# Kernel optimization log

Measured on AMD Instinct MI355X. Metric: run time of the kernel, lower is better.

The kernel has to match this reference:

```python
import jax, jax.numpy as jnp
import numpy as np

N, E, H, R, C = 20000, 640000, 256, 10, 7
B, MAXLEN = 64, 110


def setup_inputs() -> dict:
    key = jax.random.key(0)
    ks = jax.random.split(key, 12)
    return {
        "speaker": jax.random.randint(ks[0], (N,), 0, 2),
        "x": jax.random.normal(ks[1], (N, H), dtype=jnp.float32),
        "edge_index": jax.random.randint(ks[2], (2, E), 0, N),
        "edge_norm": jax.random.uniform(ks[3], (E,), dtype=jnp.float32),
        "edge_type": jax.random.randint(ks[4], (E,), 0, R),
        "seq_lengths": jax.random.randint(ks[5], (B,), 1, MAXLEN),
        "umask": jnp.ones((B, MAXLEN), dtype=jnp.float32),
        "w1": jax.random.normal(ks[6], (R, H, H), dtype=jnp.float32) * 0.02,
        "w2": jax.random.normal(ks[7], (R, H, H), dtype=jnp.float32) * 0.02,
        "lin_W": jax.random.normal(ks[8], (2 * H, H), dtype=jnp.float32) * 0.02,
        "lin_b": jnp.zeros((H,), dtype=jnp.float32),
        "fc_W": jax.random.normal(ks[9], (H, C), dtype=jnp.float32) * 0.02,
        "fc_b": jnp.zeros((C,), dtype=jnp.float32),
    }


def gnn_layer(x, w, edge_index, edge_type, edge_norm):
    # PyG MessagePassing with flow='target_to_source', aggr='mean':
    #   x_j = x[edge_index[1]], aggregate at i = edge_index[0]
    i, j = edge_index[0], edge_index[1]
    # per-edge msg = x_j @ w[edge_type]; compute as relation-batched GEMM
    xw = jnp.einsum('nd,rdo->rno', x, w)          # [R, N, H]
    msgs = xw[edge_type, j] * edge_norm[:, None]   # [E, H]
    sums = jax.ops.segment_sum(msgs, i, num_segments=x.shape[0])
    cnt = jax.ops.segment_sum(jnp.ones_like(edge_norm), i, num_segments=x.shape[0])
    return sums / jnp.maximum(cnt, 1.0)[:, None]   # scatter-mean (0 for isolated nodes)


def reference(speaker, x, edge_index, edge_norm, edge_type, seq_lengths, umask,
              w1, w2, lin_W, lin_b, fc_W, fc_b):
    en = edge_norm * 2.0  # forward passes edge_norm * 2
    # both GNN layers are type 'GGCN' -> update() returns aggr_out (GRU path is dead)
    out1 = jax.nn.sigmoid(gnn_layer(x, w1, edge_index, edge_type, en))  # dropout = eval identity
    out2 = gnn_layer(out1, w2, edge_index, edge_type, en)
    emotions = jnp.concatenate([x, out2], axis=1)            # [N, 2H]
    hidden = jax.nn.relu(emotions @ lin_W + lin_b)           # [N, H]
    logits = hidden @ fc_W + fc_b                            # [N, C]
    log_prob = jax.nn.log_softmax(logits, axis=1)
    return (log_prob, x, emotions)
```

## Files before the change

kernel.cpp:

```cpp
#include <hip/hip_runtime.h>

typedef short bf16x8 __attribute__((ext_vector_type(8)));
typedef float f32x4 __attribute__((ext_vector_type(4)));

#define RH 2560

__device__ __forceinline__ unsigned short f2bf(float f) {
  unsigned u = __float_as_uint(f);
  u += 0x7fffu + ((u >> 16) & 1u);
  return (unsigned short)(u >> 16);
}
__device__ __forceinline__ float bf2f(unsigned short s) {
  return __uint_as_float(((unsigned)s) << 16);
}

__global__ void zero_int(int* __restrict__ p, int n) {
  int i = blockIdx.x * 256 + threadIdx.x;
  if (i < n) p[i] = 0;
}
__global__ void hist_kernel(const int* __restrict__ ei, int E, int* __restrict__ cnt) {
  int e = blockIdx.x * 256 + threadIdx.x;
  if (e < E) atomicAdd(&cnt[ei[e]], 1);
}
__global__ __launch_bounds__(1024) void scan_excl(const int* __restrict__ cnt,
                                                  int* __restrict__ offs, int n) {
  __shared__ int ps[1024];
  const int t = threadIdx.x;
  const int PER = (n + 1023) >> 10;
  const int base = t * PER;
  int s = 0;
  for (int k = 0; k < PER; ++k) {
    int idx = base + k;
    if (idx < n) s += cnt[idx];
  }
  ps[t] = s;
  __syncthreads();
  for (int off = 1; off < 1024; off <<= 1) {
    int add = (t >= off) ? ps[t - off] : 0;
    __syncthreads();
    ps[t] += add;
    __syncthreads();
  }
  int run = t ? ps[t - 1] : 0;
  for (int k = 0; k < PER; ++k) {
    int idx = base + k;
    if (idx < n) { offs[idx] = run; run += cnt[idx]; }
  }
  if (t == 1023) offs[n] = run;
}
__global__ void copy_int(const int* __restrict__ a, int* __restrict__ b, int n) {
  int i = blockIdx.x * 256 + threadIdx.x;
  if (i < n) b[i] = a[i];
}
__global__ void scatter_kernel(const int* __restrict__ ei, const int* __restrict__ ejj,
                               const int* __restrict__ ety, const float* __restrict__ enm,
                               int E, int* __restrict__ cursor,
                               int* __restrict__ js, int* __restrict__ ts,
                               float* __restrict__ ns) {
  int e = blockIdx.x * 256 + threadIdx.x;
  if (e < E) {
    int s = atomicAdd(&cursor[ei[e]], 1);
    js[s] = ejj[e];
    ts[s] = ety[e];
    ns[s] = enm[e] * 2.0f;
  }
}

__global__ void packW(const float* __restrict__ w, unsigned short* __restrict__ Wt) {
  int idx = blockIdx.x * 256 + threadIdx.x;
  if (idx >= 256 * RH) return;
  int o = idx / RH;
  int k = idx - o * RH;
  Wt[idx] = f2bf(w[(size_t)k * 256 + o]);
}
__global__ void packLin(const float* __restrict__ lw, unsigned short* __restrict__ Wt) {
  int idx = blockIdx.x * 256 + threadIdx.x;
  if (idx >= 256 * 512) return;
  int o = idx >> 9;
  int k = idx & 511;
  Wt[idx] = f2bf(lw[(size_t)k * 256 + o]);
}
__global__ void copyX(const float* __restrict__ x, float* __restrict__ xcopy,
                      float* __restrict__ em, unsigned short* __restrict__ em16,
                      unsigned short* __restrict__ x16, int total) {
  int idx = blockIdx.x * 256 + threadIdx.x;
  if (idx >= total) return;
  int nrow = idx >> 8, h = idx & 255;
  float v = x[idx];
  xcopy[idx] = v;
  em[(size_t)nrow * 512 + h] = v;
  em16[(size_t)nrow * 512 + h] = f2bf(v);
  x16[idx] = f2bf(v);
}

__global__ __launch_bounds__(256) void agg_kernel2(
    const unsigned short* __restrict__ src,
    const int* __restrict__ offs,
    const int* __restrict__ js,
    const int* __restrict__ ts,
    const float* __restrict__ ns,
    unsigned short* __restrict__ S)
{
  __shared__ int sj[128];
  __shared__ int st[128];
  __shared__ float sn[128];
  __shared__ float accs[10][256];
  const int i = blockIdx.x;
  const int t = threadIdx.x;
  const int wave = t >> 6;
  const int lane = t & 63;
  const int pair = wave >> 1;
  const int wi = wave & 1;
  const int colbase = (wi * 64 + lane) * 2;
  float acc[10][2] = {};
  const int eb = offs[i], ee = offs[i + 1];
  for (int p0 = eb; p0 < ee; p0 += 128) {
    int np = min(128, ee - p0);
    __syncthreads();
    if (t < np) {
      sj[t] = js[p0 + t];
      st[t] = ts[p0 + t];
      sn[t] = ns[p0 + t];
    }
    __syncthreads();
    for (int q = pair; q < np; q += 2) {
      int jn = __builtin_amdgcn_readfirstlane(sj[q]);
      int tr = __builtin_amdgcn_readfirstlane(st[q]);
      float nr = __uint_as_float(__builtin_amdgcn_readfirstlane(__float_as_uint(sn[q])));
      unsigned v = *reinterpret_cast<const unsigned*>(src + (size_t)jn * 256 + colbase);
      float x0 = bf2f((unsigned short)(v & 0xffffu));
      float x1 = bf2f((unsigned short)(v >> 16));
#pragma unroll
      for (int r = 0; r < 10; ++r) {
        float wr = (tr == r) ? nr : 0.0f;
        acc[r][0] += wr * x0;
        acc[r][1] += wr * x1;
      }
    }
  }
  if (pair == 0) {
#pragma unroll
    for (int r = 0; r < 10; ++r) {
      accs[r][colbase] = acc[r][0];
      accs[r][colbase + 1] = acc[r][1];
    }
  }
  __syncthreads();
  if (pair == 1) {
#pragma unroll
    for (int r = 0; r < 10; ++r) {
      accs[r][colbase] += acc[r][0];
      accs[r][colbase + 1] += acc[r][1];
    }
  }
  __syncthreads();
  int cc = ee - eb;
  float scale = 1.0f / (float)(cc > 1 ? cc : 1);
  size_t base = (size_t)i * RH;
#pragma unroll
  for (int it = 0; it < 5; ++it) {
    int c = it * 512 + t * 2;
    float a0 = accs[c >> 8][c & 255] * scale;
    float a1 = accs[c >> 8][(c & 255) + 1] * scale;
    unsigned pk = (unsigned)f2bf(a0) | ((unsigned)f2bf(a1) << 16);
    *reinterpret_cast<unsigned*>(S + base + c) = pk;
  }
}

template<int MODE>
__global__ __launch_bounds__(256) void gemm128(
    const unsigned short* __restrict__ A,
    const unsigned short* __restrict__ Bt,
    int M, int K,
    float* __restrict__ fout,
    unsigned short* __restrict__ bout,
    const float* __restrict__ bias)
{
  __shared__ unsigned short At[128][40];
  __shared__ unsigned short Bs[128][40];
  const int tid = threadIdx.x;
  const int tileM = blockIdx.x * 128;
  const int tileN = blockIdx.y * 128;
  const int lane = tid & 63;
  const int wid = tid >> 6;
  const int wr = wid >> 1, wc = wid & 1;
  const int l15 = lane & 15, lq = lane >> 4;
  f32x4 acc[4][4] = {};
  const int nk = K >> 5;
  for (int kt = 0; kt < nk; ++kt) {
    __syncthreads();
#pragma unroll
    for (int p = 0; p < 2; ++p) {
      int c = tid + p * 256;
      int row = c >> 2;
      int ko = (c & 3) * 8;
      int gr = tileM + row;
      uint4 va = make_uint4(0u, 0u, 0u, 0u);
      if (gr < M) va = *reinterpret_cast<const uint4*>(A + (size_t)gr * K + kt * 32 + ko);
      *reinterpret_cast<uint4*>(&At[row][ko]) = va;
      uint4 vb = *reinterpret_cast<const uint4*>(Bt + (size_t)(tileN + row) * K + kt * 32 + ko);
      *reinterpret_cast<uint4*>(&Bs[row][ko]) = vb;
    }
    __syncthreads();
    bf16x8 af[4], bfr[4];
#pragma unroll
    for (int m = 0; m < 4; ++m)
      af[m] = *reinterpret_cast<const bf16x8*>(&At[wr * 64 + m * 16 + l15][lq * 8]);
#pragma unroll
    for (int n = 0; n < 4; ++n)
      bfr[n] = *reinterpret_cast<const bf16x8*>(&Bs[wc * 64 + n * 16 + l15][lq * 8]);
#pragma unroll
    for (int m = 0; m < 4; ++m)
#pragma unroll
      for (int n = 0; n < 4; ++n)
        acc[m][n] = __builtin_amdgcn_mfma_f32_16x16x32_bf16(af[m], bfr[n], acc[m][n], 0, 0, 0);
  }
  const int r0 = tileM + wr * 64;
  const int c0 = tileN + wc * 64;
#pragma unroll
  for (int m = 0; m < 4; ++m) {
#pragma unroll
    for (int n = 0; n < 4; ++n) {
      int col = c0 + n * 16 + l15;
      int rowb = r0 + m * 16 + lq * 4;
#pragma unroll
      for (int q = 0; q < 4; ++q) {
        int row = rowb + q;
        if (row < M) {
          float v = acc[m][n][q];
          if (MODE == 0) {
            float s = 1.0f / (1.0f + __expf(-v));
            bout[(size_t)row * 256 + col] = f2bf(s);
          } else if (MODE == 1) {
            fout[(size_t)row * 512 + col] = v;
            bout[(size_t)row * 512 + col] = f2bf(v);
          } else {
            float s = v + bias[col];
            s = s > 0.0f ? s : 0.0f;
            fout[(size_t)row * 256 + col] = s;
          }
        }
      }
    }
  }
}

__global__ __launch_bounds__(256) void fc_lsm(const float* __restrict__ hidden,
                                              const float* __restrict__ fcW,
                                              const float* __restrict__ fcb,
                                              float* __restrict__ outlp, int N) {
  __shared__ float hs[32 * 256];
  __shared__ float fw[256 * 7];
  __shared__ float lg[32][8];
  const int t = threadIdx.x;
  const int nb = blockIdx.x * 32;
  for (int c = t; c < 256 * 7; c += 256) fw[c] = fcW[c];
  for (int c = t; c < 32 * 256; c += 256) {
    int node = nb + (c >> 8);
    hs[c] = (node < N) ? hidden[(size_t)node * 256 + (c & 255)] : 0.0f;
  }
  __syncthreads();
  if (t < 224) {
    int ln = t / 7, c = t - ln * 7;
    float s = fcb[c];
    for (int h = 0; h < 256; ++h) s += hs[ln * 256 + h] * fw[h * 7 + c];
    lg[ln][c] = s;
  }
  __syncthreads();
  if (t < 32 && nb + t < N) {
    float m = lg[t][0];
    for (int c = 1; c < 7; ++c) m = fmaxf(m, lg[t][c]);
    float sum = 0.0f;
    for (int c = 0; c < 7; ++c) sum += __expf(lg[t][c] - m);
    float ls = __logf(sum);
    for (int c = 0; c < 7; ++c) outlp[(size_t)(nb + t) * 7 + c] = lg[t][c] - m - ls;
  }
}

extern "C" void kernel_launch(void* const* d_in, const int* in_sizes, int n_in,
                              void* d_out, int out_size, void* d_ws, size_t ws_size,
                              hipStream_t stream) {
  const float* x     = (const float*)d_in[1];
  const int*   ei    = (const int*)d_in[2];
  const float* enorm = (const float*)d_in[3];
  const int*   etype = (const int*)d_in[4];
  const float* w1    = (const float*)d_in[7];
  const float* w2    = (const float*)d_in[8];
  const float* linW  = (const float*)d_in[9];
  const float* linb  = (const float*)d_in[10];
  const float* fcW   = (const float*)d_in[11];
  const float* fcb   = (const float*)d_in[12];
  float* out = (float*)d_out;

  const int N = in_sizes[0];
  const int E = in_sizes[3];

  char* ws = (char*)d_ws;
  size_t off = 0;
  auto carve = [&](size_t bytes) -> void* {
    void* p = ws + off;
    off += (bytes + 255) & ~(size_t)255;
    return p;
  };
  unsigned short* S    = (unsigned short*)carve((size_t)N * RH * 2);
  unsigned short* W1t  = (unsigned short*)carve((size_t)256 * RH * 2);
  unsigned short* W2t  = (unsigned short*)carve((size_t)256 * RH * 2);
  unsigned short* LWt  = (unsigned short*)carve((size_t)256 * 512 * 2);
  unsigned short* out1 = (unsigned short*)carve((size_t)N * 256 * 2);
  unsigned short* em16 = (unsigned short*)carve((size_t)N * 512 * 2);
  unsigned short* x16  = (unsigned short*)carve((size_t)N * 256 * 2);
  int* cnt             = (int*)carve((size_t)N * 4);
  int* offs            = (int*)carve((size_t)(N + 1) * 4);
  int* cursor          = (int*)carve((size_t)N * 4);
  int* js              = (int*)carve((size_t)E * 4);
  int* ts              = (int*)carve((size_t)E * 4);
  float* ns            = (float*)carve((size_t)E * 4);
  float* hidden        = (float*)S;

  const int* e_i = ei;
  const int* e_j = ei + E;

  zero_int<<<(N + 255) / 256, 256, 0, stream>>>(cnt, N);
  hist_kernel<<<(E + 255) / 256, 256, 0, stream>>>(e_i, E, cnt);
  scan_excl<<<1, 1024, 0, stream>>>(cnt, offs, N);
  copy_int<<<(N + 255) / 256, 256, 0, stream>>>(offs, cursor, N);
  scatter_kernel<<<(E + 255) / 256, 256, 0, stream>>>(e_i, e_j, etype, enorm, E,
                                                      cursor, js, ts, ns);

  packW<<<(256 * RH + 255) / 256, 256, 0, stream>>>(w1, W1t);
  packW<<<(256 * RH + 255) / 256, 256, 0, stream>>>(w2, W2t);
  packLin<<<(256 * 512 + 255) / 256, 256, 0, stream>>>(linW, LWt);
  copyX<<<((N * 256) + 255) / 256, 256, 0, stream>>>(
      x, out + (size_t)N * 7, out + (size_t)N * 263, em16, x16, N * 256);

  dim3 gemm_grid((N + 127) / 128, 2);

  agg_kernel2<<<N, 256, 0, stream>>>(x16, offs, js, ts, ns, S);
  gemm128<0><<<gemm_grid, 256, 0, stream>>>(S, W1t, N, RH, nullptr, out1, nullptr);

  agg_kernel2<<<N, 256, 0, stream>>>(out1, offs, js, ts, ns, S);
  gemm128<1><<<gemm_grid, 256, 0, stream>>>(S, W2t, N, RH,
      out + (size_t)N * 263 + 256, em16 + 256, nullptr);

  gemm128<2><<<gemm_grid, 256, 0, stream>>>(em16, LWt, N, 512, hidden, nullptr, linb);

  fc_lsm<<<(N + 31) / 32, 256, 0, stream>>>(hidden, fcW, fcb, out, N);
}
```

Before: 641.3 us.

## Bucket edges by (node, relation) and aggregate one node per wave

Edges are now sorted into CSR buckets keyed by node*10+relation, with the source index and normalised weight packed into one int2. The aggregation kernel gives each wave one node and walks the relation buckets in turn, so every lane accumulates 4 columns without shared memory, barriers or a per-edge 10-way select. This removes the redundant multiply-adds across all relations and the block-level reduction. In exchange the histogram, scan and cursor arrays grow tenfold, which makes the single-block scan longer, and the work per wave varies with node degree.

```diff
diff --git a/kernel.cpp b/kernel.cpp
--- a/kernel.cpp
+++ b/kernel.cpp
@@ -18,9 +18,10 @@
   int i = blockIdx.x * 256 + threadIdx.x;
   if (i < n) p[i] = 0;
 }
-__global__ void hist_kernel(const int* __restrict__ ei, int E, int* __restrict__ cnt) {
+__global__ void hist_kernel(const int* __restrict__ ei, const int* __restrict__ ety,
+                            int E, int* __restrict__ cnt) {
   int e = blockIdx.x * 256 + threadIdx.x;
-  if (e < E) atomicAdd(&cnt[ei[e]], 1);
+  if (e < E) atomicAdd(&cnt[ei[e] * 10 + ety[e]], 1);
 }
 __global__ __launch_bounds__(1024) void scan_excl(const int* __restrict__ cnt,
                                                   int* __restrict__ offs, int n) {
@@ -54,15 +55,11 @@
 }
 __global__ void scatter_kernel(const int* __restrict__ ei, const int* __restrict__ ejj,
                                const int* __restrict__ ety, const float* __restrict__ enm,
-                               int E, int* __restrict__ cursor,
-                               int* __restrict__ js, int* __restrict__ ts,
-                               float* __restrict__ ns) {
+                               int E, int* __restrict__ cursor, int2* __restrict__ jnpk) {
   int e = blockIdx.x * 256 + threadIdx.x;
   if (e < E) {
-    int s = atomicAdd(&cursor[ei[e]], 1);
-    js[s] = ejj[e];
-    ts[s] = ety[e];
-    ns[s] = enm[e] * 2.0f;
+    int s = atomicAdd(&cursor[ei[e] * 10 + ety[e]], 1);
+    jnpk[s] = make_int2(ejj[e], __float_as_int(enm[e] * 2.0f));
   }
 }
 
@@ -93,77 +90,44 @@
   x16[idx] = f2bf(v);
 }
 
-__global__ __launch_bounds__(256) void agg_kernel2(
+__global__ __launch_bounds__(256) void agg_kernel3(
     const unsigned short* __restrict__ src,
-    const int* __restrict__ offs,
-    const int* __restrict__ js,
-    const int* __restrict__ ts,
-    const float* __restrict__ ns,
-    unsigned short* __restrict__ S)
+    const int* __restrict__ offs2,
+    const int2* __restrict__ jnpk,
+    unsigned short* __restrict__ S, int N)
 {
-  __shared__ int sj[128];
-  __shared__ int st[128];
-  __shared__ float sn[128];
-  __shared__ float accs[10][256];
-  const int i = blockIdx.x;
-  const int t = threadIdx.x;
-  const int wave = t >> 6;
-  const int lane = t & 63;
-  const int pair = wave >> 1;
-  const int wi = wave & 1;
-  const int colbase = (wi * 64 + lane) * 2;
-  float acc[10][2] = {};
-  const int eb = offs[i], ee = offs[i + 1];
-  for (int p0 = eb; p0 < ee; p0 += 128) {
-    int np = min(128, ee - p0);
-    __syncthreads();
-    if (t < np) {
-      sj[t] = js[p0 + t];
-      st[t] = ts[p0 + t];
-      sn[t] = ns[p0 + t];
+  const int wave = threadIdx.x >> 6;
+  const int lane = threadIdx.x & 63;
+  const int node = blockIdx.x * 4 + wave;
+  if (node >= N) return;
+  const int b10 = node * 10;
+  const int cb = lane * 4;
+  float a0[10], a1[10], a2[10], a3[10];
+#pragma unroll
+  for (int r = 0; r < 10; ++r) {
+    int sb = offs2[b10 + r];
+    int se = offs2[b10 + r + 1];
+    float b0 = 0.f, b1 = 0.f, b2 = 0.f, b3 = 0.f;
+    for (int q = sb; q < se; ++q) {
+      int2 jn = jnpk[q];
+      float nr = __int_as_float(jn.y);
+      uint2 v = *reinterpret_cast<const uint2*>(src + (size_t)jn.x * 256 + cb);
+      b0 += nr * __uint_as_float(v.x << 16);
+      b1 += nr * __uint_as_float(v.x & 0xffff0000u);
+      b2 += nr * __uint_as_float(v.y << 16);
+      b3 += nr * __uint_as_float(v.y & 0xffff0000u);
     }
-    __syncthreads();
-    for (int q = pair; q < np; q += 2) {
-      int jn = __builtin_amdgcn_readfirstlane(sj[q]);
-      int tr = __builtin_amdgcn_readfirstlane(st[q]);
-      float nr = __uint_as_float(__builtin_amdgcn_readfirstlane(__float_as_uint(sn[q])));
-      unsigned v = *reinterpret_cast<const unsigned*>(src + (size_t)jn * 256 + colbase);
-      float x0 = bf2f((unsigned short)(v & 0xffffu));
-      float x1 = bf2f((unsigned short)(v >> 16));
-#pragma unroll
-      for (int r = 0; r < 10; ++r) {
-        float wr = (tr == r) ? nr : 0.0f;
-        acc[r][0] += wr * x0;
-        acc[r][1] += wr * x1;
-      }
-    }
-  }
-  if (pair == 0) {
-#pragma unroll
-    for (int r = 0; r < 10; ++r) {
-      accs[r][colbase] = acc[r][0];
-      accs[r][colbase + 1] = acc[r][1];
-    }
-  }
-  __syncthreads();
-  if (pair == 1) {
-#pragma unroll
-    for (int r = 0; r < 10; ++r) {
-      accs[r][colbase] += acc[r][0];
-      accs[r][colbase + 1] += acc[r][1];
-    }
-  }
-  __syncthreads();
-  int cc = ee - eb;
+    a0[r] = b0; a1[r] = b1; a2[r] = b2; a3[r] = b3;
+  }
+  int cc = offs2[b10 + 10] - offs2[b10];
   float scale = 1.0f / (float)(cc > 1 ? cc : 1);
-  size_t base = (size_t)i * RH;
-#pragma unroll
-  for (int it = 0; it < 5; ++it) {
-    int c = it * 512 + t * 2;
-    float a0 = accs[c >> 8][c & 255] * scale;
-    float a1 = accs[c >> 8][(c & 255) + 1] * scale;
-    unsigned pk = (unsigned)f2bf(a0) | ((unsigned)f2bf(a1) << 16);
-    *reinterpret_cast<unsigned*>(S + base + c) = pk;
+  size_t base = (size_t)node * RH + cb;
+#pragma unroll
+  for (int r = 0; r < 10; ++r) {
+    unsigned p0 = (unsigned)f2bf(a0[r] * scale) | ((unsigned)f2bf(a1[r] * scale) << 16);
+    unsigned p1 = (unsigned)f2bf(a2[r] * scale) | ((unsigned)f2bf(a3[r] * scale) << 16);
+    uint2 pk; pk.x = p0; pk.y = p1;
+    *reinterpret_cast<uint2*>(S + base + r * 256) = pk;
   }
 }
 
@@ -294,6 +258,7 @@
 
   const int N = in_sizes[0];
   const int E = in_sizes[3];
+  const int NB = N * 10;
 
   char* ws = (char*)d_ws;
   size_t off = 0;
@@ -309,23 +274,21 @@
   unsigned short* out1 = (unsigned short*)carve((size_t)N * 256 * 2);
   unsigned short* em16 = (unsigned short*)carve((size_t)N * 512 * 2);
   unsigned short* x16  = (unsigned short*)carve((size_t)N * 256 * 2);
-  int* cnt             = (int*)carve((size_t)N * 4);
-  int* offs            = (int*)carve((size_t)(N + 1) * 4);
-  int* cursor          = (int*)carve((size_t)N * 4);
-  int* js              = (int*)carve((size_t)E * 4);
-  int* ts              = (int*)carve((size_t)E * 4);
-  float* ns            = (float*)carve((size_t)E * 4);
+  int* cnt2            = (int*)carve((size_t)NB * 4);
+  int* offs2           = (int*)carve((size_t)(NB + 1) * 4);
+  int* cursor          = (int*)carve((size_t)NB * 4);
+  int2* jnpk           = (int2*)carve((size_t)E * 8);
   float* hidden        = (float*)S;
 
   const int* e_i = ei;
   const int* e_j = ei + E;
 
-  zero_int<<<(N + 255) / 256, 256, 0, stream>>>(cnt, N);
-  hist_kernel<<<(E + 255) / 256, 256, 0, stream>>>(e_i, E, cnt);
-  scan_excl<<<1, 1024, 0, stream>>>(cnt, offs, N);
-  copy_int<<<(N + 255) / 256, 256, 0, stream>>>(offs, cursor, N);
+  zero_int<<<(NB + 255) / 256, 256, 0, stream>>>(cnt2, NB);
+  hist_kernel<<<(E + 255) / 256, 256, 0, stream>>>(e_i, etype, E, cnt2);
+  scan_excl<<<1, 1024, 0, stream>>>(cnt2, offs2, NB);
+  copy_int<<<(NB + 255) / 256, 256, 0, stream>>>(offs2, cursor, NB);
   scatter_kernel<<<(E + 255) / 256, 256, 0, stream>>>(e_i, e_j, etype, enorm, E,
-                                                      cursor, js, ts, ns);
+                                                      cursor, jnpk);
 
   packW<<<(256 * RH + 255) / 256, 256, 0, stream>>>(w1, W1t);
   packW<<<(256 * RH + 255) / 256, 256, 0, stream>>>(w2, W2t);
@@ -335,10 +298,10 @@
 
   dim3 gemm_grid((N + 127) / 128, 2);
 
-  agg_kernel2<<<N, 256, 0, stream>>>(x16, offs, js, ts, ns, S);
+  agg_kernel3<<<(N + 3) / 4, 256, 0, stream>>>(x16, offs2, jnpk, S, N);
   gemm128<0><<<gemm_grid, 256, 0, stream>>>(S, W1t, N, RH, nullptr, out1, nullptr);
 
-  agg_kernel2<<<N, 256, 0, stream>>>(out1, offs, js, ts, ns, S);
+  agg_kernel3<<<(N + 3) / 4, 256, 0, stream>>>(out1, offs2, jnpk, S, N);
   gemm128<1><<<gemm_grid, 256, 0, stream>>>(S, W2t, N, RH,
       out + (size_t)N * 263 + 256, em16 + 256, nullptr);
 
```

After: 939.0 us. +46.4%, slower.
